# Performance work log

Hardware: AMD Instinct MI355X
Metric: run time of the kernel (lower is better)

## Reference

```python
import jax, jax.numpy as jnp
import numpy as np

N, M, D, OUT, K, L = 2048, 64, 64, 64, 3, 3  # meta-nodes, subgraph-nodes, channels, out, hops, layers
EPS = 1e-5


def setup_inputs() -> dict:
    key = jax.random.key(0)
    ks = jax.random.split(key, 6)
    x = jax.random.normal(ks[0], (N, M, D), dtype=jnp.float32)
    adj = jax.random.randint(ks[1], (N, N), 0, 2, dtype=jnp.int32)        # meta-graph adjacency
    sub_adj = jax.random.randint(ks[2], (M, M), 0, 2, dtype=jnp.int32)    # per-node subgraph adjacency
    # GCNConv params: (num_layers, k+1 convs per layer, D, D)
    W_convs = jax.random.normal(ks[3], (L, K + 1, D, D), dtype=jnp.float32) / np.float32(np.sqrt(D))
    b_convs = jnp.zeros((L, K + 1, D), dtype=jnp.float32)
    # LayerNorm over the trailing (m, d) dims, per layer
    ln_gamma = jnp.ones((L, M, D), dtype=jnp.float32)
    ln_beta = jnp.zeros((L, M, D), dtype=jnp.float32)
    W_lin = jax.random.normal(ks[4], (M * D, OUT), dtype=jnp.float32) / np.float32(np.sqrt(M * D))
    b_lin = jnp.zeros((OUT,), dtype=jnp.float32)
    return dict(x=x, sub_adj=sub_adj, adj=adj, W_convs=W_convs, b_convs=b_convs,
                ln_gamma=ln_gamma, ln_beta=ln_beta, W_lin=W_lin, b_lin=b_lin)


def _gcn_norm(A):
    # symmetric GCN normalization with self loops: D^{-1/2} (A+I) D^{-1/2}
    A = A.astype(jnp.float32) + jnp.eye(A.shape[0], dtype=jnp.float32)
    dinv = jax.lax.rsqrt(A.sum(axis=1))  # degree >= 1 thanks to self loops
    return dinv[:, None] * A * dinv[None, :]


def reference(x, sub_adj, adj, W_convs, b_convs, ln_gamma, ln_beta, W_lin, b_lin):
    # precompute_adj: dense powers [A, A^2, ..., A^K] of the meta-graph adjacency
    A = adj.astype(jnp.float32)
    cached = [A]
    P = A
    for _ in range(K - 1):
        P = P @ A
        cached.append(P)

    Sn = _gcn_norm(sub_adj)  # (M, M) shared normalized subgraph propagation

    def gcn(h, W, b):
        # GCNConv over the subgraph (m) dimension: Sn @ (h W) + b, batched over n
        return jnp.einsum('uv,nvd->nud', Sn, h @ W) + b

    for l in range(L):
        h = gcn(x, W_convs[l, 0], b_convs[l, 0])  # L[0](x, sub_adj)
        x_i = x
        for i in range(K):
            # k-hop propagation over the meta graph: x_i <- A^i-power @ x_i
            x_i = jnp.einsum('nj,jmd->nmd', cached[i], x_i)
            h = h + gcn(x_i, W_convs[l, i + 1], b_convs[l, i + 1])
        # LayerNorm over trailing (m, d) dims, then ReLU
        mu = h.mean(axis=(1, 2), keepdims=True)
        var = h.var(axis=(1, 2), keepdims=True)
        x = (h - mu) * jax.lax.rsqrt(var + EPS) * ln_gamma[l] + ln_beta[l]
        x = jax.nn.relu(x)

    # final readout linear over flattened (m*d)
    out = x.reshape(N, M * D) @ W_lin + b_lin  # (N, OUT)
    return out
```

## Files before the change

kernel.cpp:

```cpp
#include <hip/hip_runtime.h>
#include <math.h>

#define NN 2048
#define MM 64
#define DD 64
#define MD 4096
#define NLAYER 3
#define EPS 1e-5f

typedef unsigned short u16;
typedef unsigned int u32;
typedef __attribute__((ext_vector_type(8))) short bf16x8;
typedef __attribute__((ext_vector_type(4))) float f32x4;

__device__ inline u16 f32_to_bf16(float f) {
    u32 u = __float_as_uint(f);
    u32 r = (u + 0x7FFFu + ((u >> 16) & 1u)) >> 16;
    return (u16)r;
}
__device__ inline float bf16_to_f32(u16 h) { return __uint_as_float((u32)h << 16); }

__global__ __launch_bounds__(256) void aprep_kernel(const int* __restrict__ adj,
                                                    u16* __restrict__ Abf,
                                                    u16* __restrict__ ATbf) {
    __shared__ u16 T[64][65];
    const int r0 = blockIdx.y * 64, c0 = blockIdx.x * 64;
    const int tid = threadIdx.x;
#pragma unroll
    for (int e = 0; e < 16; ++e) {
        int idx = e * 256 + tid;
        int i = idx >> 6, j = idx & 63;
        int a = adj[(long)(r0 + i) * NN + c0 + j];
        u16 b = a ? (u16)0x3F80 : (u16)0;
        Abf[(long)(r0 + i) * NN + c0 + j] = b;
        T[i][j] = b;
    }
    __syncthreads();
#pragma unroll
    for (int e = 0; e < 16; ++e) {
        int idx = e * 256 + tid;
        int cc = idx >> 6, rr = idx & 63;
        ATbf[(long)(c0 + cc) * NN + r0 + rr] = T[rr][cc];
    }
}

__global__ __launch_bounds__(256) void sn_kernel(const int* __restrict__ sub,
                                                 float* __restrict__ Sn) {
    __shared__ float dinv[64];
    int tid = threadIdx.x;
    if (tid < 64) {
        float s = 1.f;
        for (int v = 0; v < 64; ++v) s += (float)sub[tid * 64 + v];
        dinv[tid] = 1.f / sqrtf(s);
    }
    __syncthreads();
    for (int t = tid; t < 4096; t += 256) {
        int u = t >> 6, v = t & 63;
        float a = (float)sub[t] + (u == v ? 1.f : 0.f);
        Sn[t] = dinv[u] * a * dinv[v];
    }
}

template <int S>
__global__ __launch_bounds__(256) void split_pow_kernel(const float* __restrict__ X,
                                                        u16* __restrict__ P, long n) {
    long i = (long)blockIdx.x * 256 + threadIdx.x;
    if (i >= n) return;
    float v = X[i];
#pragma unroll
    for (int s = 0; s < S; ++s) {
        u16 h = f32_to_bf16(v);
        P[(long)s * n + i] = h;
        v -= bf16_to_f32(h);
    }
}

__global__ __launch_bounds__(256) void split3t_kernel(const float* __restrict__ X,
                                                      u16* __restrict__ P, int R, int Cc) {
    __shared__ float T[64][65];
    const int r0 = blockIdx.y * 64, c0 = blockIdx.x * 64;
    const int tid = threadIdx.x;
#pragma unroll
    for (int e = 0; e < 16; ++e) {
        int idx = e * 256 + tid;
        int i = idx >> 6, j = idx & 63;
        T[i][j] = X[(long)(r0 + i) * Cc + c0 + j];
    }
    __syncthreads();
    const long planeStride = (long)R * Cc;
#pragma unroll
    for (int e = 0; e < 16; ++e) {
        int idx = e * 256 + tid;
        int cc = idx >> 6, rr = idx & 63;
        float v = T[rr][cc];
        u16 h = f32_to_bf16(v);
        float r1 = v - bf16_to_f32(h);
        u16 lo = f32_to_bf16(r1);
        float r2 = r1 - bf16_to_f32(lo);
        u16 ll = f32_to_bf16(r2);
        long o = (long)(c0 + cc) * R + r0 + rr;
        P[o] = h;
        P[planeStride + o] = lo;
        P[2 * planeStride + o] = ll;
    }
}

template <int SP, int SQ, int SMAX>
__global__ __launch_bounds__(256) void gemm_pairs(const u16* __restrict__ Ap, long aStride,
                                                  const u16* __restrict__ Bp, long bStride,
                                                  float* __restrict__ C, int M, int N, int K) {
    __shared__ u16 lds[(SP + SQ) * 4096];
    const int tid = threadIdx.x;
    const int wave = tid >> 6, lane = tid & 63;
    const int bm = blockIdx.y * 128, bn = blockIdx.x * 128;
    const int wr = (wave >> 1) * 64, wc = (wave & 1) * 64;

    f32x4 acc[4][4];
#pragma unroll
    for (int i = 0; i < 4; ++i)
#pragma unroll
        for (int j = 0; j < 4; ++j) acc[i][j] = (f32x4){0.f, 0.f, 0.f, 0.f};

    const int kb16 = lane >> 4, lr = lane & 15;
    int aoff[4], boff[4];
#pragma unroll
    for (int mi = 0; mi < 4; ++mi) {
        int ua = (wr + mi * 16 + lr) * 4 + kb16;
        aoff[mi] = (ua ^ ((ua >> 3) & 7)) * 16;
        int ub = (wc + mi * 16 + lr) * 4 + kb16;
        boff[mi] = (ub ^ ((ub >> 3) & 7)) * 16;
    }
    for (int k0 = 0; k0 < K; k0 += 32) {
#pragma unroll
        for (int u8 = 0; u8 < (SP + SQ) * 2; ++u8) {
            int uu = u8 * 4 + wave;
            int p = uu >> 3, i = uu & 7;
            int us = i * 64 + lane;
            int ulin = us ^ ((us >> 3) & 7);
            int r = ulin >> 2, kb = ulin & 3;
            const u16* src;
            int rowbase;
            if (p < SP) { src = Ap + (long)p * aStride; rowbase = bm; }
            else        { src = Bp + (long)(p - SP) * bStride; rowbase = bn; }
            const char* g = (const char*)src + ((long)(rowbase + r) * K + k0) * 2 + kb * 16;
            char* l = (char*)lds + p * 8192 + i * 1024 + lane * 16;
            __builtin_amdgcn_global_load_lds((const __attribute__((address_space(1))) void*)g,
                                             (__attribute__((address_space(3))) void*)l, 16, 0, 0);
        }
        __syncthreads();
        bf16x8 a[SP][4], b[SQ][4];
#pragma unroll
        for (int s = 0; s < SP; ++s)
#pragma unroll
            for (int mi = 0; mi < 4; ++mi)
                a[s][mi] = *(const bf16x8*)((const char*)lds + s * 8192 + aoff[mi]);
#pragma unroll
        for (int t = 0; t < SQ; ++t)
#pragma unroll
            for (int ni = 0; ni < 4; ++ni)
                b[t][ni] = *(const bf16x8*)((const char*)lds + (SP + t) * 8192 + boff[ni]);
#pragma unroll
        for (int s = 0; s < SP; ++s)
#pragma unroll
            for (int t = 0; t < SQ; ++t)
                if (s + t <= SMAX) {
#pragma unroll
                    for (int mi = 0; mi < 4; ++mi)
#pragma unroll
                        for (int ni = 0; ni < 4; ++ni)
                            acc[mi][ni] = __builtin_amdgcn_mfma_f32_16x16x32_bf16(
                                a[s][mi], b[t][ni], acc[mi][ni], 0, 0, 0);
                }
        __syncthreads();
    }
#pragma unroll
    for (int mi = 0; mi < 4; ++mi)
#pragma unroll
        for (int ni = 0; ni < 4; ++ni)
#pragma unroll
            for (int j = 0; j < 4; ++j)
                C[(long)(bm + wr + mi * 16 + (lane >> 4) * 4 + j) * N + bn + wc + ni * 16 + lr] =
                    acc[mi][ni][j];
}

__global__ __launch_bounds__(256) void gcn_kernel(const float* __restrict__ Xin,
                                                  const float* __restrict__ W,
                                                  const float* __restrict__ bias,
                                                  const float* __restrict__ Sn,
                                                  float* __restrict__ H, int accum) {
    __shared__ float Xs[64][65];
    __shared__ float Ws[64][65];
    __shared__ float Ts[64][65];
    const int n = blockIdx.x;
    const int tid = threadIdx.x;
    const float* Xn = Xin + (size_t)n * MD;
    for (int t = tid; t < 4096; t += 256) {
        int r = t >> 6, c = t & 63;
        Xs[r][c] = Xn[t];
        Ws[r][c] = W[t];
    }
    __syncthreads();
    const int tx = tid & 15, ty = tid >> 4;
    float acc[4][4] = {};
#pragma unroll 8
    for (int k = 0; k < 64; ++k) {
        float a0 = Xs[ty * 4 + 0][k], a1 = Xs[ty * 4 + 1][k];
        float a2 = Xs[ty * 4 + 2][k], a3 = Xs[ty * 4 + 3][k];
        float b0 = Ws[k][tx * 4 + 0], b1 = Ws[k][tx * 4 + 1];
        float b2 = Ws[k][tx * 4 + 2], b3 = Ws[k][tx * 4 + 3];
        acc[0][0] += a0 * b0; acc[0][1] += a0 * b1; acc[0][2] += a0 * b2; acc[0][3] += a0 * b3;
        acc[1][0] += a1 * b0; acc[1][1] += a1 * b1; acc[1][2] += a1 * b2; acc[1][3] += a1 * b3;
        acc[2][0] += a2 * b0; acc[2][1] += a2 * b1; acc[2][2] += a2 * b2; acc[2][3] += a2 * b3;
        acc[3][0] += a3 * b0; acc[3][1] += a3 * b1; acc[3][2] += a3 * b2; acc[3][3] += a3 * b3;
    }
#pragma unroll
    for (int i = 0; i < 4; ++i)
#pragma unroll
        for (int j = 0; j < 4; ++j) Ts[ty * 4 + i][tx * 4 + j] = acc[i][j];
    __syncthreads();
    float acc2[4][4] = {};
#pragma unroll 8
    for (int v = 0; v < 64; ++v) {
        float a0 = Sn[(ty * 4 + 0) * 64 + v], a1 = Sn[(ty * 4 + 1) * 64 + v];
        float a2 = Sn[(ty * 4 + 2) * 64 + v], a3 = Sn[(ty * 4 + 3) * 64 + v];
        float b0 = Ts[v][tx * 4 + 0], b1 = Ts[v][tx * 4 + 1];
        float b2 = Ts[v][tx * 4 + 2], b3 = Ts[v][tx * 4 + 3];
        acc2[0][0] += a0 * b0; acc2[0][1] += a0 * b1; acc2[0][2] += a0 * b2; acc2[0][3] += a0 * b3;
        acc2[1][0] += a1 * b0; acc2[1][1] += a1 * b1; acc2[1][2] += a1 * b2; acc2[1][3] += a1 * b3;
        acc2[2][0] += a2 * b0; acc2[2][1] += a2 * b1; acc2[2][2] += a2 * b2; acc2[2][3] += a2 * b3;
        acc2[3][0] += a3 * b0; acc2[3][1] += a3 * b1; acc2[3][2] += a3 * b2; acc2[3][3] += a3 * b3;
    }
    float* Hn = H + (size_t)n * MD;
#pragma unroll
    for (int i = 0; i < 4; ++i)
#pragma unroll
        for (int j = 0; j < 4; ++j) {
            int idx = (ty * 4 + i) * 64 + tx * 4 + j;
            float val = acc2[i][j] + bias[tx * 4 + j];
            Hn[idx] = accum ? (Hn[idx] + val) : val;
        }
}

__global__ __launch_bounds__(256) void ln_relu_kernel(const float* __restrict__ H,
                                                      const float* __restrict__ gamma,
                                                      const float* __restrict__ beta,
                                                      float* __restrict__ X) {
    const int n = blockIdx.x;
    const int tid = threadIdx.x;
    const float* h = H + (size_t)n * MD;
    __shared__ float wsum[4], wsum2[4];
    float s = 0.f;
    for (int t = tid; t < MD; t += 256) s += h[t];
#pragma unroll
    for (int o = 32; o; o >>= 1) s += __shfl_down(s, o);
    if ((tid & 63) == 0) wsum[tid >> 6] = s;
    __syncthreads();
    float mean = (wsum[0] + wsum[1] + wsum[2] + wsum[3]) * (1.f / 4096.f);
    float v2 = 0.f;
    for (int t = tid; t < MD; t += 256) { float d = h[t] - mean; v2 += d * d; }
#pragma unroll
    for (int o = 32; o; o >>= 1) v2 += __shfl_down(v2, o);
    if ((tid & 63) == 0) wsum2[tid >> 6] = v2;
    __syncthreads();
    float var = (wsum2[0] + wsum2[1] + wsum2[2] + wsum2[3]) * (1.f / 4096.f);
    float rstd = 1.f / sqrtf(var + EPS);
    float* xo = X + (size_t)n * MD;
    for (int t = tid; t < MD; t += 256) {
        float val = (h[t] - mean) * rstd * gamma[t] + beta[t];
        xo[t] = val > 0.f ? val : 0.f;
    }
}

__global__ __launch_bounds__(256) void readout_kernel(const float* __restrict__ X,
                                                      const float* __restrict__ Wl,
                                                      const float* __restrict__ bl,
                                                      float* __restrict__ out) {
    const int n = blockIdx.x;
    const int o = threadIdx.x & 63, c = threadIdx.x >> 6;
    const float* xn = X + (size_t)n * MD;
    float s = 0.f;
    for (int i = c * 1024; i < (c + 1) * 1024; ++i) s += xn[i] * Wl[(size_t)i * 64 + o];
    __shared__ float red[4][64];
    red[c][o] = s;
    __syncthreads();
    if (c == 0) out[(size_t)n * 64 + o] = red[0][o] + red[1][o] + red[2][o] + red[3][o] + bl[o];
}

extern "C" void kernel_launch(void* const* d_in, const int* in_sizes, int n_in,
                              void* d_out, int out_size, void* d_ws, size_t ws_size,
                              hipStream_t stream) {
    const float* x     = (const float*)d_in[0];
    const int*   sub   = (const int*)d_in[1];
    const int*   adj   = (const int*)d_in[2];
    const float* Wc    = (const float*)d_in[3];
    const float* bc    = (const float*)d_in[4];
    const float* gamma = (const float*)d_in[5];
    const float* beta  = (const float*)d_in[6];
    const float* Wlin  = (const float*)d_in[7];
    const float* blin  = (const float*)d_in[8];
    float* out = (float*)d_out;

    char* w = (char*)d_ws;
    u16* Abf = (u16*)w;  w += (size_t)NN * NN * 2;
    u16* A2p = (u16*)w;  w += (size_t)2 * NN * NN * 2;
    u16* A3p = (u16*)w;  w += (size_t)3 * NN * NN * 2;
    float* Sn = (float*)w; w += (size_t)4096 * 4;
    u16* S = (u16*)w;    w += (size_t)3 * NN * MD * 2;
    float* Xp = (float*)w; w += (size_t)NN * MD * 4;
    float* H  = (float*)w; w += (size_t)NN * MD * 4;
    u16* ATbf = S;
    float* A2f = (float*)((char*)S + (size_t)NN * NN * 2);
    float* A3f = (float*)((char*)A2f + (size_t)NN * NN * 4);

    aprep_kernel<<<dim3(32, 32), 256, 0, stream>>>(adj, Abf, ATbf);
    sn_kernel<<<1, 256, 0, stream>>>(sub, Sn);
    gemm_pairs<1, 1, 2><<<dim3(16, 16), 256, 0, stream>>>(Abf, 0, ATbf, 0, A2f, NN, NN, NN);
    split_pow_kernel<2><<<(NN * NN + 255) / 256, 256, 0, stream>>>(A2f, A2p, (long)NN * NN);
    gemm_pairs<2, 1, 2><<<dim3(16, 16), 256, 0, stream>>>(A2p, (long)NN * NN, ATbf, 0, A3f, NN, NN, NN);
    split_pow_kernel<3><<<(NN * NN + 255) / 256, 256, 0, stream>>>(A3f, A3p, (long)NN * NN);

    const float* xin = x;
    for (int l = 0; l < NLAYER; ++l) {
        const float* Wl = Wc + (size_t)l * 4 * 4096;
        const float* bl = bc + (size_t)l * 4 * 64;
        split3t_kernel<<<dim3(64, 32), 256, 0, stream>>>(xin, S, NN, MD);
        gcn_kernel<<<NN, 256, 0, stream>>>(xin, Wl, bl, Sn, H, 0);
        gemm_pairs<1, 3, 2><<<dim3(32, 16), 256, 0, stream>>>(Abf, 0, S, (long)NN * MD, Xp, NN, MD, NN);
        gcn_kernel<<<NN, 256, 0, stream>>>(Xp, Wl + 4096, bl + 64, Sn, H, 1);
        split3t_kernel<<<dim3(64, 32), 256, 0, stream>>>(Xp, S, NN, MD);
        gemm_pairs<2, 3, 2><<<dim3(32, 16), 256, 0, stream>>>(A2p, (long)NN * NN, S, (long)NN * MD, Xp, NN, MD, NN);
        gcn_kernel<<<NN, 256, 0, stream>>>(Xp, Wl + 2 * 4096, bl + 2 * 64, Sn, H, 1);
        split3t_kernel<<<dim3(64, 32), 256, 0, stream>>>(Xp, S, NN, MD);
        gemm_pairs<3, 3, 2><<<dim3(32, 16), 256, 0, stream>>>(A3p, (long)NN * NN, S, (long)NN * MD, Xp, NN, MD, NN);
        gcn_kernel<<<NN, 256, 0, stream>>>(Xp, Wl + 3 * 4096, bl + 3 * 64, Sn, H, 1);
        ln_relu_kernel<<<NN, 256, 0, stream>>>(H, gamma + (size_t)l * 4096,
                                               beta + (size_t)l * 4096, H);
        xin = H;
    }
    readout_kernel<<<NN, 256, 0, stream>>>(H, Wlin, blin, out);
}
```

Baseline: 2.170 ms.

## Fuse GCN convs with LayerNorm on MFMA, add GEMM prefetch and block swizzle

Moves the per-node GCN convolutions from scalar FP32 FMA onto bf16x3 split MFMA, with W and Sn pre-split into swizzled bf16 planes. When the workspace is large enough, all four convs of a layer plus LayerNorm/ReLU run in one kernel over four stored hop outputs. This removes repeated H read-modify-write passes and the separate LN kernel. The hop GEMM also gets single-buffer prefetch of the next K tile, overlapping loads with MFMA, and a block-index swizzle for cache locality. The bf16x3 split uses 6 of the 9 term products, which may slightly change precision compared with FP32 FMA.

```diff
diff --git a/kernel.cpp b/kernel.cpp
--- a/kernel.cpp
+++ b/kernel.cpp
@@ -19,6 +19,11 @@
     return (u16)r;
 }
 __device__ inline float bf16_to_f32(u16 h) { return __uint_as_float((u32)h << 16); }
+__device__ inline void split3(float f, u16& h, u16& l, u16& q) {
+    h = f32_to_bf16(f); float r = f - bf16_to_f32(h);
+    l = f32_to_bf16(r); r -= bf16_to_f32(l);
+    q = f32_to_bf16(r);
+}
 
 __global__ __launch_bounds__(256) void aprep_kernel(const int* __restrict__ adj,
                                                     u16* __restrict__ Abf,
@@ -44,9 +49,10 @@
     }
 }
 
-__global__ __launch_bounds__(256) void sn_kernel(const int* __restrict__ sub,
-                                                 float* __restrict__ Sn) {
+__global__ __launch_bounds__(256) void snprep_kernel(const int* __restrict__ sub,
+                                                     u16* __restrict__ SnS) {
     __shared__ float dinv[64];
+    __shared__ float Snl[64][65];
     int tid = threadIdx.x;
     if (tid < 64) {
         float s = 1.f;
@@ -57,7 +63,40 @@
     for (int t = tid; t < 4096; t += 256) {
         int u = t >> 6, v = t & 63;
         float a = (float)sub[t] + (u == v ? 1.f : 0.f);
-        Sn[t] = dinv[u] * a * dinv[v];
+        Snl[u][v] = dinv[u] * a * dinv[v];
+    }
+    __syncthreads();
+    for (int u = tid * 2; u < tid * 2 + 2; ++u) {
+        int row = u >> 3, c8 = u & 7;
+        int su = (u ^ ((u >> 3) & 7)) * 8;
+#pragma unroll
+        for (int e = 0; e < 8; ++e) {
+            u16 h, l, q; split3(Snl[row][c8 * 8 + e], h, l, q);
+            SnS[su + e] = h;
+            SnS[4096 + su + e] = l;
+            SnS[8192 + su + e] = q;
+        }
+    }
+}
+
+__global__ __launch_bounds__(256) void wprep_kernel(const float* __restrict__ Wc,
+                                                    u16* __restrict__ WtS) {
+    __shared__ float Wl[64][65];
+    const int cu = blockIdx.x, tid = threadIdx.x;
+    const float* W = Wc + (size_t)cu * 4096;
+    for (int t = tid; t < 4096; t += 256) Wl[t >> 6][t & 63] = W[t];
+    __syncthreads();
+    u16* dst = WtS + (size_t)cu * 3 * 4096;
+    for (int u = tid * 2; u < tid * 2 + 2; ++u) {
+        int d = u >> 3, c8 = u & 7;
+        int su = (u ^ ((u >> 3) & 7)) * 8;
+#pragma unroll
+        for (int e = 0; e < 8; ++e) {
+            u16 h, l, q; split3(Wl[c8 * 8 + e][d], h, l, q);
+            dst[su + e] = h;
+            dst[4096 + su + e] = l;
+            dst[8192 + su + e] = q;
+        }
     }
 }
 
@@ -93,15 +132,11 @@
         int idx = e * 256 + tid;
         int cc = idx >> 6, rr = idx & 63;
         float v = T[rr][cc];
-        u16 h = f32_to_bf16(v);
-        float r1 = v - bf16_to_f32(h);
-        u16 lo = f32_to_bf16(r1);
-        float r2 = r1 - bf16_to_f32(lo);
-        u16 ll = f32_to_bf16(r2);
+        u16 h, l, q; split3(v, h, l, q);
         long o = (long)(c0 + cc) * R + r0 + rr;
         P[o] = h;
-        P[planeStride + o] = lo;
-        P[2 * planeStride + o] = ll;
+        P[planeStride + o] = l;
+        P[2 * planeStride + o] = q;
     }
 }
 
@@ -112,7 +147,10 @@
     __shared__ u16 lds[(SP + SQ) * 4096];
     const int tid = threadIdx.x;
     const int wave = tid >> 6, lane = tid & 63;
-    const int bm = blockIdx.y * 128, bn = blockIdx.x * 128;
+    const int nwg = gridDim.x * gridDim.y;
+    int bid = blockIdx.y * gridDim.x + blockIdx.x;
+    int sbid = (bid & 7) * (nwg >> 3) + (bid >> 3);
+    const int bm = (sbid / gridDim.x) * 128, bn = (sbid % gridDim.x) * 128;
     const int wr = (wave >> 1) * 64, wc = (wave & 1) * 64;
 
     f32x4 acc[4][4];
@@ -130,7 +168,7 @@
         int ub = (wc + mi * 16 + lr) * 4 + kb16;
         boff[mi] = (ub ^ ((ub >> 3) & 7)) * 16;
     }
-    for (int k0 = 0; k0 < K; k0 += 32) {
+    auto stage = [&](int k0) {
 #pragma unroll
         for (int u8 = 0; u8 < (SP + SQ) * 2; ++u8) {
             int uu = u8 * 4 + wave;
@@ -138,8 +176,7 @@
             int us = i * 64 + lane;
             int ulin = us ^ ((us >> 3) & 7);
             int r = ulin >> 2, kb = ulin & 3;
-            const u16* src;
-            int rowbase;
+            const u16* src; int rowbase;
             if (p < SP) { src = Ap + (long)p * aStride; rowbase = bm; }
             else        { src = Bp + (long)(p - SP) * bStride; rowbase = bn; }
             const char* g = (const char*)src + ((long)(rowbase + r) * K + k0) * 2 + kb * 16;
@@ -147,7 +184,10 @@
             __builtin_amdgcn_global_load_lds((const __attribute__((address_space(1))) void*)g,
                                              (__attribute__((address_space(3))) void*)l, 16, 0, 0);
         }
-        __syncthreads();
+    };
+    stage(0);
+    __syncthreads();
+    for (int k0 = 0; k0 < K; k0 += 32) {
         bf16x8 a[SP][4], b[SQ][4];
 #pragma unroll
         for (int s = 0; s < SP; ++s)
@@ -159,6 +199,8 @@
 #pragma unroll
             for (int ni = 0; ni < 4; ++ni)
                 b[t][ni] = *(const bf16x8*)((const char*)lds + (SP + t) * 8192 + boff[ni]);
+        __syncthreads();
+        if (k0 + 32 < K) stage(k0 + 32);
 #pragma unroll
         for (int s = 0; s < SP; ++s)
 #pragma unroll
@@ -183,92 +225,184 @@
                     acc[mi][ni][j];
 }
 
-__global__ __launch_bounds__(256) void gcn_kernel(const float* __restrict__ Xin,
-                                                  const float* __restrict__ W,
-                                                  const float* __restrict__ bias,
-                                                  const float* __restrict__ Sn,
-                                                  float* __restrict__ H, int accum) {
-    __shared__ float Xs[64][65];
-    __shared__ float Ws[64][65];
-    __shared__ float Ts[64][65];
+template <int NC, int MODE>
+__global__ __launch_bounds__(256, 2) void gcn_conv_kernel(
+    const float* __restrict__ X0, const float* __restrict__ X1,
+    const float* __restrict__ X2, const float* __restrict__ X3,
+    const u16* __restrict__ WtS,
+    const float* __restrict__ bias,
+    const u16* __restrict__ SnS,
+    const float* __restrict__ gam, const float* __restrict__ bet,
+    float* __restrict__ Hout) {
+    __shared__ u16 lds[9 * 4096];
+    __shared__ float redf[4];
+    const int tid = threadIdx.x;
+    const int wave = tid >> 6, lane = tid & 63;
+    const int lr = lane & 15, lg = lane >> 4;
     const int n = blockIdx.x;
-    const int tid = threadIdx.x;
-    const float* Xn = Xin + (size_t)n * MD;
-    for (int t = tid; t < 4096; t += 256) {
-        int r = t >> 6, c = t & 63;
-        Xs[r][c] = Xn[t];
-        Ws[r][c] = W[t];
-    }
-    __syncthreads();
-    const int tx = tid & 15, ty = tid >> 4;
-    float acc[4][4] = {};
-#pragma unroll 8
-    for (int k = 0; k < 64; ++k) {
-        float a0 = Xs[ty * 4 + 0][k], a1 = Xs[ty * 4 + 1][k];
-        float a2 = Xs[ty * 4 + 2][k], a3 = Xs[ty * 4 + 3][k];
-        float b0 = Ws[k][tx * 4 + 0], b1 = Ws[k][tx * 4 + 1];
-        float b2 = Ws[k][tx * 4 + 2], b3 = Ws[k][tx * 4 + 3];
-        acc[0][0] += a0 * b0; acc[0][1] += a0 * b1; acc[0][2] += a0 * b2; acc[0][3] += a0 * b3;
-        acc[1][0] += a1 * b0; acc[1][1] += a1 * b1; acc[1][2] += a1 * b2; acc[1][3] += a1 * b3;
-        acc[2][0] += a2 * b0; acc[2][1] += a2 * b1; acc[2][2] += a2 * b2; acc[2][3] += a2 * b3;
-        acc[3][0] += a3 * b0; acc[3][1] += a3 * b1; acc[3][2] += a3 * b2; acc[3][3] += a3 * b3;
-    }
-#pragma unroll
-    for (int i = 0; i < 4; ++i)
-#pragma unroll
-        for (int j = 0; j < 4; ++j) Ts[ty * 4 + i][tx * 4 + j] = acc[i][j];
-    __syncthreads();
-    float acc2[4][4] = {};
-#pragma unroll 8
-    for (int v = 0; v < 64; ++v) {
-        float a0 = Sn[(ty * 4 + 0) * 64 + v], a1 = Sn[(ty * 4 + 1) * 64 + v];
-        float a2 = Sn[(ty * 4 + 2) * 64 + v], a3 = Sn[(ty * 4 + 3) * 64 + v];
-        float b0 = Ts[v][tx * 4 + 0], b1 = Ts[v][tx * 4 + 1];
-        float b2 = Ts[v][tx * 4 + 2], b3 = Ts[v][tx * 4 + 3];
-        acc2[0][0] += a0 * b0; acc2[0][1] += a0 * b1; acc2[0][2] += a0 * b2; acc2[0][3] += a0 * b3;
-        acc2[1][0] += a1 * b0; acc2[1][1] += a1 * b1; acc2[1][2] += a1 * b2; acc2[1][3] += a1 * b3;
-        acc2[2][0] += a2 * b0; acc2[2][1] += a2 * b1; acc2[2][2] += a2 * b2; acc2[2][3] += a2 * b3;
-        acc2[3][0] += a3 * b0; acc2[3][1] += a3 * b1; acc2[3][2] += a3 * b2; acc2[3][3] += a3 * b3;
-    }
-    float* Hn = H + (size_t)n * MD;
-#pragma unroll
-    for (int i = 0; i < 4; ++i)
+    const int TT = 0, WT = 3 * 4096, SN = 6 * 4096;
+
+    {
+        const char* src = (const char*)SnS;
+        char* dst = (char*)lds + (size_t)SN * 2;
+#pragma unroll
+        for (int i = 0; i < 6; ++i)
+            __builtin_amdgcn_global_load_lds(
+                (const __attribute__((address_space(1))) void*)(src + (i * 256 + tid) * 16),
+                (__attribute__((address_space(3))) void*)(dst + (i * 256 + tid) * 16), 16, 0, 0);
+    }
+    const float* Xc[4] = {X0, X1, X2, X3};
+    f32x4 accH[4];
+#pragma unroll
+    for (int ni = 0; ni < 4; ++ni) accH[ni] = (f32x4){0.f, 0.f, 0.f, 0.f};
+
+    for (int c = 0; c < NC; ++c) {
+        __syncthreads();
+        {
+            const char* wsrc = (const char*)(WtS + (size_t)c * 3 * 4096);
+            char* wdst = (char*)lds + (size_t)WT * 2;
+#pragma unroll
+            for (int i = 0; i < 6; ++i)
+                __builtin_amdgcn_global_load_lds(
+                    (const __attribute__((address_space(1))) void*)(wsrc + (i * 256 + tid) * 16),
+                    (__attribute__((address_space(3))) void*)(wdst + (i * 256 + tid) * 16), 16, 0, 0);
+        }
+        const float* xp = Xc[c] + (size_t)n * 4096;
+        bf16x8 xb[3][4][2];
+#pragma unroll
+        for (int ni = 0; ni < 4; ++ni)
+#pragma unroll
+            for (int ks = 0; ks < 2; ++ks) {
+                int off = (ni * 16 + lr) * 64 + ks * 32 + lg * 8;
+                f32x4 v0 = *(const f32x4*)(xp + off);
+                f32x4 v1 = *(const f32x4*)(xp + off + 4);
+#pragma unroll
+                for (int e = 0; e < 8; ++e) {
+                    float f = (e < 4) ? v0[e] : v1[e - 4];
+                    u16 h, l, q; split3(f, h, l, q);
+                    xb[0][ni][ks][e] = (short)h;
+                    xb[1][ni][ks][e] = (short)l;
+                    xb[2][ni][ks][e] = (short)q;
+                }
+            }
+        __syncthreads();
+        f32x4 accT[4];
+#pragma unroll
+        for (int ni = 0; ni < 4; ++ni) accT[ni] = (f32x4){0.f, 0.f, 0.f, 0.f};
+#pragma unroll
+        for (int ks = 0; ks < 2; ++ks) {
+            bf16x8 aw[3];
+#pragma unroll
+            for (int s = 0; s < 3; ++s) {
+                int u = (wave * 16 + lr) * 8 + ks * 4 + lg;
+                aw[s] = *(const bf16x8*)(lds + WT + s * 4096 + (u ^ ((u >> 3) & 7)) * 8);
+            }
+#pragma unroll
+            for (int ni = 0; ni < 4; ++ni) {
+                accT[ni] = __builtin_amdgcn_mfma_f32_16x16x32_bf16(aw[0], xb[0][ni][ks], accT[ni], 0, 0, 0);
+                accT[ni] = __builtin_amdgcn_mfma_f32_16x16x32_bf16(aw[0], xb[1][ni][ks], accT[ni], 0, 0, 0);
+                accT[ni] = __builtin_amdgcn_mfma_f32_16x16x32_bf16(aw[1], xb[0][ni][ks], accT[ni], 0, 0, 0);
+                accT[ni] = __builtin_amdgcn_mfma_f32_16x16x32_bf16(aw[1], xb[1][ni][ks], accT[ni], 0, 0, 0);
+                accT[ni] = __builtin_amdgcn_mfma_f32_16x16x32_bf16(aw[2], xb[0][ni][ks], accT[ni], 0, 0, 0);
+                accT[ni] = __builtin_amdgcn_mfma_f32_16x16x32_bf16(aw[0], xb[2][ni][ks], accT[ni], 0, 0, 0);
+            }
+        }
+#pragma unroll
+        for (int ni = 0; ni < 4; ++ni)
+#pragma unroll
+            for (int j = 0; j < 4; ++j) {
+                int d = wave * 16 + lg * 4 + j;
+                int v = ni * 16 + lr;
+                u16 h, l, q; split3(accT[ni][j], h, l, q);
+                int u = d * 8 + (v >> 3);
+                int o = (u ^ ((u >> 3) & 7)) * 8 + (v & 7);
+                lds[TT + o] = h;
+                lds[TT + 4096 + o] = l;
+                lds[TT + 8192 + o] = q;
+            }
+        __syncthreads();
+#pragma unroll
+        for (int ks = 0; ks < 2; ++ks) {
+            bf16x8 as_[3];
+#pragma unroll
+            for (int s = 0; s < 3; ++s) {
+                int u = (wave * 16 + lr) * 8 + ks * 4 + lg;
+                as_[s] = *(const bf16x8*)(lds + SN + s * 4096 + (u ^ ((u >> 3) & 7)) * 8);
+            }
+#pragma unroll
+            for (int ni = 0; ni < 4; ++ni) {
+                bf16x8 bt[3];
+#pragma unroll
+                for (int t = 0; t < 3; ++t) {
+                    int u = (ni * 16 + lr) * 8 + ks * 4 + lg;
+                    bt[t] = *(const bf16x8*)(lds + TT + t * 4096 + (u ^ ((u >> 3) & 7)) * 8);
+                }
+                accH[ni] = __builtin_amdgcn_mfma_f32_16x16x32_bf16(as_[0], bt[0], accH[ni], 0, 0, 0);
+                accH[ni] = __builtin_amdgcn_mfma_f32_16x16x32_bf16(as_[0], bt[1], accH[ni], 0, 0, 0);
+                accH[ni] = __builtin_amdgcn_mfma_f32_16x16x32_bf16(as_[1], bt[0], accH[ni], 0, 0, 0);
+                accH[ni] = __builtin_amdgcn_mfma_f32_16x16x32_bf16(as_[1], bt[1], accH[ni], 0, 0, 0);
+                accH[ni] = __builtin_amdgcn_mfma_f32_16x16x32_bf16(as_[2], bt[0], accH[ni], 0, 0, 0);
+                accH[ni] = __builtin_amdgcn_mfma_f32_16x16x32_bf16(as_[0], bt[2], accH[ni], 0, 0, 0);
+            }
+        }
+#pragma unroll
+        for (int ni = 0; ni < 4; ++ni) {
+            float bv = bias[c * 64 + ni * 16 + lr];
+            accH[ni][0] += bv; accH[ni][1] += bv; accH[ni][2] += bv; accH[ni][3] += bv;
+        }
+    }
+    float* hp = Hout + (size_t)n * 4096;
+    float val[4][4];
+#pragma unroll
+    for (int ni = 0; ni < 4; ++ni)
 #pragma unroll
         for (int j = 0; j < 4; ++j) {
-            int idx = (ty * 4 + i) * 64 + tx * 4 + j;
-            float val = acc2[i][j] + bias[tx * 4 + j];
-            Hn[idx] = accum ? (Hn[idx] + val) : val;
-        }
-}
-
-__global__ __launch_bounds__(256) void ln_relu_kernel(const float* __restrict__ H,
-                                                      const float* __restrict__ gamma,
-                                                      const float* __restrict__ beta,
-                                                      float* __restrict__ X) {
-    const int n = blockIdx.x;
-    const int tid = threadIdx.x;
-    const float* h = H + (size_t)n * MD;
-    __shared__ float wsum[4], wsum2[4];
-    float s = 0.f;
-    for (int t = tid; t < MD; t += 256) s += h[t];
-#pragma unroll
-    for (int o = 32; o; o >>= 1) s += __shfl_down(s, o);
-    if ((tid & 63) == 0) wsum[tid >> 6] = s;
-    __syncthreads();
-    float mean = (wsum[0] + wsum[1] + wsum[2] + wsum[3]) * (1.f / 4096.f);
-    float v2 = 0.f;
-    for (int t = tid; t < MD; t += 256) { float d = h[t] - mean; v2 += d * d; }
-#pragma unroll
-    for (int o = 32; o; o >>= 1) v2 += __shfl_down(v2, o);
-    if ((tid & 63) == 0) wsum2[tid >> 6] = v2;
-    __syncthreads();
-    float var = (wsum2[0] + wsum2[1] + wsum2[2] + wsum2[3]) * (1.f / 4096.f);
+            int idx = (wave * 16 + lg * 4 + j) * 64 + ni * 16 + lr;
+            float v = accH[ni][j];
+            if (MODE == 0 || MODE == 2) v += hp[idx];
+            val[ni][j] = v;
+        }
+    if (MODE == 0 || MODE == 1) {
+#pragma unroll
+        for (int ni = 0; ni < 4; ++ni)
+#pragma unroll
+            for (int j = 0; j < 4; ++j)
+                hp[(wave * 16 + lg * 4 + j) * 64 + ni * 16 + lr] = val[ni][j];
+        return;
+    }
+    float part = 0.f;
+#pragma unroll
+    for (int ni = 0; ni < 4; ++ni)
+#pragma unroll
+        for (int j = 0; j < 4; ++j) part += val[ni][j];
+#pragma unroll
+    for (int o = 32; o; o >>= 1) part += __shfl_down(part, o);
+    if (lane == 0) redf[wave] = part;
+    __syncthreads();
+    float mean = (redf[0] + redf[1] + redf[2] + redf[3]) * (1.f / 4096.f);
+    float p2 = 0.f;
+#pragma unroll
+    for (int ni = 0; ni < 4; ++ni)
+#pragma unroll
+        for (int j = 0; j < 4; ++j) {
+            float d_ = val[ni][j] - mean;
+            p2 += d_ * d_;
+        }
+#pragma unroll
+    for (int o = 32; o; o >>= 1) p2 += __shfl_down(p2, o);
+    __syncthreads();
+    if (lane == 0) redf[wave] = p2;
+    __syncthreads();
+    float var = (redf[0] + redf[1] + redf[2] + redf[3]) * (1.f / 4096.f);
     float rstd = 1.f / sqrtf(var + EPS);
-    float* xo = X + (size_t)n * MD;
-    for (int t = tid; t < MD; t += 256) {
-        float val = (h[t] - mean) * rstd * gamma[t] + beta[t];
-        xo[t] = val > 0.f ? val : 0.f;
-    }
+#pragma unroll
+    for (int ni = 0; ni < 4; ++ni)
+#pragma unroll
+        for (int j = 0; j < 4; ++j) {
+            int idx = (wave * 16 + lg * 4 + j) * 64 + ni * 16 + lr;
+            float v = (val[ni][j] - mean) * rstd * gam[idx] + bet[idx];
+            hp[idx] = v > 0.f ? v : 0.f;
+        }
 }
 
 __global__ __launch_bounds__(256) void readout_kernel(const float* __restrict__ X,
@@ -304,38 +438,68 @@
     u16* Abf = (u16*)w;  w += (size_t)NN * NN * 2;
     u16* A2p = (u16*)w;  w += (size_t)2 * NN * NN * 2;
     u16* A3p = (u16*)w;  w += (size_t)3 * NN * NN * 2;
-    float* Sn = (float*)w; w += (size_t)4096 * 4;
-    u16* S = (u16*)w;    w += (size_t)3 * NN * MD * 2;
-    float* Xp = (float*)w; w += (size_t)NN * MD * 4;
-    float* H  = (float*)w; w += (size_t)NN * MD * 4;
+    u16* SnS = (u16*)w;  w += (size_t)3 * 4096 * 2;
+    u16* WtS = (u16*)w;  w += (size_t)12 * 3 * 4096 * 2;
+    u16* S   = (u16*)w;  w += (size_t)3 * NN * MD * 2;
+    const size_t baseBytes = (size_t)(w - (char*)d_ws);
+    const size_t ybytes = (size_t)NN * MD * 4;
+    const bool fused = ws_size >= baseBytes + 4 * ybytes;
     u16* ATbf = S;
     float* A2f = (float*)((char*)S + (size_t)NN * NN * 2);
     float* A3f = (float*)((char*)A2f + (size_t)NN * NN * 4);
 
     aprep_kernel<<<dim3(32, 32), 256, 0, stream>>>(adj, Abf, ATbf);
-    sn_kernel<<<1, 256, 0, stream>>>(sub, Sn);
+    snprep_kernel<<<1, 256, 0, stream>>>(sub, SnS);
+    wprep_kernel<<<12, 256, 0, stream>>>(Wc, WtS);
     gemm_pairs<1, 1, 2><<<dim3(16, 16), 256, 0, stream>>>(Abf, 0, ATbf, 0, A2f, NN, NN, NN);
     split_pow_kernel<2><<<(NN * NN + 255) / 256, 256, 0, stream>>>(A2f, A2p, (long)NN * NN);
     gemm_pairs<2, 1, 2><<<dim3(16, 16), 256, 0, stream>>>(A2p, (long)NN * NN, ATbf, 0, A3f, NN, NN, NN);
     split_pow_kernel<3><<<(NN * NN + 255) / 256, 256, 0, stream>>>(A3f, A3p, (long)NN * NN);
 
-    const float* xin = x;
-    for (int l = 0; l < NLAYER; ++l) {
-        const float* Wl = Wc + (size_t)l * 4 * 4096;
-        const float* bl = bc + (size_t)l * 4 * 64;
-        split3t_kernel<<<dim3(64, 32), 256, 0, stream>>>(xin, S, NN, MD);
-        gcn_kernel<<<NN, 256, 0, stream>>>(xin, Wl, bl, Sn, H, 0);
-        gemm_pairs<1, 3, 2><<<dim3(32, 16), 256, 0, stream>>>(Abf, 0, S, (long)NN * MD, Xp, NN, MD, NN);
-        gcn_kernel<<<NN, 256, 0, stream>>>(Xp, Wl + 4096, bl + 64, Sn, H, 1);
-        split3t_kernel<<<dim3(64, 32), 256, 0, stream>>>(Xp, S, NN, MD);
-        gemm_pairs<2, 3, 2><<<dim3(32, 16), 256, 0, stream>>>(A2p, (long)NN * NN, S, (long)NN * MD, Xp, NN, MD, NN);
-        gcn_kernel<<<NN, 256, 0, stream>>>(Xp, Wl + 2 * 4096, bl + 2 * 64, Sn, H, 1);
-        split3t_kernel<<<dim3(64, 32), 256, 0, stream>>>(Xp, S, NN, MD);
-        gemm_pairs<3, 3, 2><<<dim3(32, 16), 256, 0, stream>>>(A3p, (long)NN * NN, S, (long)NN * MD, Xp, NN, MD, NN);
-        gcn_kernel<<<NN, 256, 0, stream>>>(Xp, Wl + 3 * 4096, bl + 3 * 64, Sn, H, 1);
-        ln_relu_kernel<<<NN, 256, 0, stream>>>(H, gamma + (size_t)l * 4096,
-                                               beta + (size_t)l * 4096, H);
-        xin = H;
-    }
-    readout_kernel<<<NN, 256, 0, stream>>>(H, Wlin, blin, out);
-}
+    const dim3 gp(32, 16);
+    if (fused) {
+        float* Y[4];
+        for (int i = 0; i < 4; ++i) { Y[i] = (float*)w; w += ybytes; }
+        const float* xin = x;
+        for (int l = 0; l < NLAYER; ++l) {
+            float* p1 = Y[l % 4];
+            float* p2 = Y[(l + 1) % 4];
+            float* p3 = Y[(l + 2) % 4];
+            const u16* Wl = WtS + (size_t)l * 12 * 4096;
+            split3t_kernel<<<dim3(64, 32), 256, 0, stream>>>(xin, S, NN, MD);
+            gemm_pairs<1, 3, 2><<<gp, 256, 0, stream>>>(Abf, 0, S, (long)NN * MD, p1, NN, MD, NN);
+            split3t_kernel<<<dim3(64, 32), 256, 0, stream>>>(p1, S, NN, MD);
+            gemm_pairs<2, 3, 2><<<gp, 256, 0, stream>>>(A2p, (long)NN * NN, S, (long)NN * MD, p2, NN, MD, NN);
+            split3t_kernel<<<dim3(64, 32), 256, 0, stream>>>(p2, S, NN, MD);
+            gemm_pairs<3, 3, 2><<<gp, 256, 0, stream>>>(A3p, (long)NN * NN, S, (long)NN * MD, p3, NN, MD, NN);
+            gcn_conv_kernel<4, 3><<<NN, 256, 0, stream>>>(xin, p1, p2, p3, Wl,
+                bc + (size_t)l * 256, SnS, gamma + (size_t)l * 4096, beta + (size_t)l * 4096, p1);
+            xin = p1;
+        }
+        readout_kernel<<<NN, 256, 0, stream>>>(xin, Wlin, blin, out);
+    } else {
+        float* Xp = (float*)w; w += ybytes;
+        float* H  = (float*)w; w += ybytes;
+        const float* xin = x;
+        for (int l = 0; l < NLAYER; ++l) {
+            const u16* Wl = WtS + (size_t)l * 12 * 4096;
+            const float* bl = bc + (size_t)l * 256;
+            split3t_kernel<<<dim3(64, 32), 256, 0, stream>>>(xin, S, NN, MD);
+            gemm_pairs<1, 3, 2><<<gp, 256, 0, stream>>>(Abf, 0, S, (long)NN * MD, Xp, NN, MD, NN);
+            gcn_conv_kernel<1, 1><<<NN, 256, 0, stream>>>(xin, xin, xin, xin, Wl, bl,
+                SnS, nullptr, nullptr, H);
+            gcn_conv_kernel<1, 0><<<NN, 256, 0, stream>>>(Xp, Xp, Xp, Xp, Wl + 3 * 4096, bl + 64,
+                SnS, nullptr, nullptr, H);
+            split3t_kernel<<<dim3(64, 32), 256, 0, stream>>>(Xp, S, NN, MD);
+            gemm_pairs<2, 3, 2><<<gp, 256, 0, stream>>>(A2p, (long)NN * NN, S, (long)NN * MD, Xp, NN, MD, NN);
+            gcn_conv_kernel<1, 0><<<NN, 256, 0, stream>>>(Xp, Xp, Xp, Xp, Wl + 6 * 4096, bl + 128,
+                SnS, nullptr, nullptr, H);
+            split3t_kernel<<<dim3(64, 32), 256, 0, stream>>>(Xp, S, NN, MD);
+            gemm_pairs<3, 3, 2><<<gp, 256, 0, stream>>>(A3p, (long)NN * NN, S, (long)NN * MD, Xp, NN, MD, NN);
+            gcn_conv_kernel<1, 2><<<NN, 256, 0, stream>>>(Xp, Xp, Xp, Xp, Wl + 9 * 4096, bl + 192,
+                SnS, gamma + (size_t)l * 4096, beta + (size_t)l * 4096, H);
+            xin = H;
+        }
+        readout_kernel<<<NN, 256, 0, stream>>>(xin, Wlin, blin, out);
+    }
+}
```

New measurement: 1.963 ms. 9.5% less time.
